# Optimization experiments

Measured on AMD Instinct MI355X. Metric: run time of the kernel, lower is better.

The kernel has to match this reference:

```python
import jax, jax.numpy as jnp
import numpy as np

# SMPL kinematic tree: parent[i] for joint i (root's parent is -1, unused)
PARENTS = [-1, 0, 0, 0, 1, 2, 3, 4, 5, 6, 7, 8, 9, 9, 9, 12, 13, 14, 16, 17, 18, 19, 20, 21]
NUM_JOINTS = 24
NUM_VERTS = 6890
BATCH = 128


def rodrigues(r):
    """r: [K,3] axis-angle -> [K,3,3] rotation (faithful to source, incl. cos(theta*pi)/sin(theta))."""
    eps = 1e-8
    theta = jnp.linalg.norm(r + eps, axis=-1, keepdims=True)  # [K,1]
    r_hat = r / theta                                          # [K,3]
    cos = jnp.cos(theta * jnp.pi)[..., None]                   # [K,1,1]
    sin = jnp.sin(theta)[..., None]                            # [K,1,1]
    rx, ry, rz = r_hat[:, 0], r_hat[:, 1], r_hat[:, 2]
    z = jnp.zeros_like(rx)
    m = jnp.stack([z, -rz, ry, rz, z, -rx, -ry, rx, z], axis=1).reshape(-1, 3, 3)
    eye = jnp.eye(3, dtype=r.dtype)
    dot = r_hat[:, :, None] * r_hat[:, None, :]                # outer product [K,3,3]
    return cos * eye + (1.0 - cos) * dot + sin * m


def setup_inputs() -> dict:
    key = jax.random.key(0)
    k1, k2, k3, k4 = jax.random.split(key, 4)
    V = jax.random.normal(k1, (BATCH, NUM_VERTS, 3), dtype=jnp.float32)
    J = jax.random.normal(k2, (BATCH, NUM_JOINTS, 3), dtype=jnp.float32)
    pose = jax.random.normal(k3, (BATCH, NUM_JOINTS, 3), dtype=jnp.float32)
    W = jax.random.uniform(k4, (BATCH, NUM_VERTS, NUM_JOINTS), dtype=jnp.float32)
    return {"V": V, "J": J, "pose": pose, "W": W}


def reference(V, J, pose, W):
    B = V.shape[0]
    M = NUM_JOINTS
    R = rodrigues(pose.reshape(-1, 3)).reshape(B, M, 3, 3)     # [B,M,3,3]
    # local translations: root uses J[0], others J[i] - J[parent[i]]
    par = np.array(PARENTS[1:])
    t = jnp.concatenate([J[:, :1], J[:, 1:] - J[:, par]], axis=1)  # [B,M,3]
    bottom = jnp.broadcast_to(jnp.array([0.0, 0.0, 0.0, 1.0], dtype=V.dtype), (B, M, 1, 4))
    A = jnp.concatenate([jnp.concatenate([R, t[..., None]], axis=-1), bottom], axis=2)  # [B,M,4,4]
    # forward kinematics along the tree (fixed 24-joint loop; parents always precede children)
    results = [A[:, 0]]
    for i in range(1, M):
        results.append(jnp.matmul(results[PARENTS[i]], A[:, i]))
    G = jnp.stack(results, axis=1)                              # [B,M,4,4]
    # subtract transformed rest-pose joint locations (the 'pack' correction)
    Jh = jnp.concatenate([J, jnp.zeros((B, M, 1), dtype=V.dtype)], axis=-1)  # [B,M,4]
    corr = jnp.einsum('bmij,bmj->bmi', G, Jh)                   # [B,M,4]
    Gc = G - jnp.concatenate([jnp.zeros((B, M, 4, 3), dtype=V.dtype), corr[..., None]], axis=-1)
    # linear blend skinning, without materializing [B,N,M,4,4]
    Tv = jnp.einsum('bnm,bmij->bnij', W, Gc)                    # [B,N,4,4]
    Vh = jnp.concatenate([V, jnp.ones((B, V.shape[1], 1), dtype=V.dtype)], axis=-1)  # [B,N,4]
    out = jnp.einsum('bnij,bnj->bni', Tv, Vh)                   # [B,N,4]
    return out[:, :, :3]
```

## Files before the change

### kernel.cpp

```cpp
#include <hip/hip_runtime.h>
#include <math.h>

#define NJ 24
#define NV 6890
#define NB 128

__constant__ int d_anc[NJ][8] = {
  {-1,-1,-1,-1,-1,-1,-1,-1},
  { 0,-1,-1,-1,-1,-1,-1,-1},
  { 0,-1,-1,-1,-1,-1,-1,-1},
  { 0,-1,-1,-1,-1,-1,-1,-1},
  { 1, 0,-1,-1,-1,-1,-1,-1},
  { 2, 0,-1,-1,-1,-1,-1,-1},
  { 3, 0,-1,-1,-1,-1,-1,-1},
  { 4, 1, 0,-1,-1,-1,-1,-1},
  { 5, 2, 0,-1,-1,-1,-1,-1},
  { 6, 3, 0,-1,-1,-1,-1,-1},
  { 7, 4, 1, 0,-1,-1,-1,-1},
  { 8, 5, 2, 0,-1,-1,-1,-1},
  { 9, 6, 3, 0,-1,-1,-1,-1},
  { 9, 6, 3, 0,-1,-1,-1,-1},
  { 9, 6, 3, 0,-1,-1,-1,-1},
  {12, 9, 6, 3, 0,-1,-1,-1},
  {13, 9, 6, 3, 0,-1,-1,-1},
  {14, 9, 6, 3, 0,-1,-1,-1},
  {16,13, 9, 6, 3, 0,-1,-1},
  {17,14, 9, 6, 3, 0,-1,-1},
  {18,16,13, 9, 6, 3, 0,-1},
  {19,17,14, 9, 6, 3, 0,-1},
  {20,18,16,13, 9, 6, 3, 0},
  {21,19,17,14, 9, 6, 3, 0}
};
__constant__ int d_par[NJ] = {-1,0,0,0,1,2,3,4,5,6,7,8,9,9,9,12,13,14,16,17,18,19,20,21};

__global__ __launch_bounds__(64) void chain_kernel(const float* __restrict__ J,
                                                   const float* __restrict__ pose,
                                                   float* __restrict__ Gc) {
    int b = blockIdx.x;
    int tid = threadIdx.x;
    __shared__ float A[NJ][12];

    if (tid < NJ) {
        int i = tid;
        const float* p = pose + ((size_t)b * NJ + i) * 3;
        float rx = p[0], ry = p[1], rz = p[2];
        float ex = rx + 1e-8f, ey = ry + 1e-8f, ez = rz + 1e-8f;
        float theta = sqrtf(ex * ex + ey * ey + ez * ez);
        float inv = 1.0f / theta;
        float hx = rx * inv, hy = ry * inv, hz = rz * inv;
        float c = cosf(theta * (float)M_PI);
        float s = sinf(theta);
        float oc = 1.0f - c;
        const float* jp = J + ((size_t)b * NJ + i) * 3;
        int par = d_par[i];
        float tx, ty, tz;
        if (par < 0) {
            tx = jp[0]; ty = jp[1]; tz = jp[2];
        } else {
            const float* jq = J + ((size_t)b * NJ + par) * 3;
            tx = jp[0] - jq[0]; ty = jp[1] - jq[1]; tz = jp[2] - jq[2];
        }
        A[i][0]  = c + oc * hx * hx;
        A[i][1]  = oc * hx * hy - s * hz;
        A[i][2]  = oc * hx * hz + s * hy;
        A[i][3]  = tx;
        A[i][4]  = oc * hy * hx + s * hz;
        A[i][5]  = c + oc * hy * hy;
        A[i][6]  = oc * hy * hz - s * hx;
        A[i][7]  = ty;
        A[i][8]  = oc * hz * hx - s * hy;
        A[i][9]  = oc * hz * hy + s * hx;
        A[i][10] = c + oc * hz * hz;
        A[i][11] = tz;
    }
    __syncthreads();

    if (tid < NJ) {
        int i = tid;
        float M[12];
        #pragma unroll
        for (int j = 0; j < 12; j++) M[j] = A[i][j];

        for (int k = 0; k < 8; k++) {
            int p = d_anc[i][k];
            if (p < 0) break;
            float P[12];
            #pragma unroll
            for (int j = 0; j < 12; j++) P[j] = A[p][j];
            float N[12];
            #pragma unroll
            for (int r = 0; r < 3; r++) {
                float p0 = P[r*4+0], p1 = P[r*4+1], p2 = P[r*4+2], p3 = P[r*4+3];
                N[r*4+0] = p0 * M[0] + p1 * M[4] + p2 * M[8];
                N[r*4+1] = p0 * M[1] + p1 * M[5] + p2 * M[9];
                N[r*4+2] = p0 * M[2] + p1 * M[6] + p2 * M[10];
                N[r*4+3] = p0 * M[3] + p1 * M[7] + p2 * M[11] + p3;
            }
            #pragma unroll
            for (int j = 0; j < 12; j++) M[j] = N[j];
        }

        const float* jp = J + ((size_t)b * NJ + i) * 3;
        float jx = jp[0], jy = jp[1], jz = jp[2];
        float* o = Gc + ((size_t)b * NJ + i) * 12;
        #pragma unroll
        for (int r = 0; r < 3; r++) {
            float g0 = M[r*4+0], g1 = M[r*4+1], g2 = M[r*4+2], g3 = M[r*4+3];
            float corr = g0 * jx + g1 * jy + g2 * jz;
            o[r*4+0] = g0;
            o[r*4+1] = g1;
            o[r*4+2] = g2;
            o[r*4+3] = g3 - corr;
        }
    }
}

typedef __attribute__((ext_vector_type(16))) float fx16;

__global__ __launch_bounds__(256) void lbs_kernel(const float* __restrict__ V,
                                                  const float* __restrict__ W,
                                                  const float* __restrict__ Gc,
                                                  float* __restrict__ out) {
    const int b = blockIdx.y;
    const int n = blockIdx.x * 256 + threadIdx.x;
    if (n >= NV) return;

    const float* gb = Gc + (size_t)b * (NJ * 12);

    const float4* wp = (const float4*)(W + ((size_t)b * NV + n) * 24);
    float4 warr[6];
    #pragma unroll
    for (int k = 0; k < 6; k++) warr[k] = wp[k];

    float T[12];
    #pragma unroll
    for (int j = 0; j < 12; j++) T[j] = 0.0f;

    #pragma unroll
    for (int c = 0; c < 6; c++) {
        fx16 ga, gB, gC;
        const float* p = gb + c * 48;
        asm volatile("s_load_dwordx16 %0, %3, 0x0\n\t"
                     "s_load_dwordx16 %1, %3, 0x40\n\t"
                     "s_load_dwordx16 %2, %3, 0x80\n\t"
                     "s_waitcnt lgkmcnt(0)"
                     : "=&s"(ga), "=&s"(gB), "=&s"(gC)
                     : "s"(p));

        const float wm[4] = {warr[c].x, warr[c].y, warr[c].z, warr[c].w};
        #pragma unroll
        for (int q = 0; q < 4; q++) {
            float wq = wm[q];
            #pragma unroll
            for (int j = 0; j < 12; j++) {
                const int flat = q * 12 + j;
                float g = (flat < 16) ? ga[flat < 16 ? flat : 0]
                        : (flat < 32) ? gB[flat >= 16 && flat < 32 ? flat - 16 : 0]
                                      : gC[flat >= 32 ? flat - 32 : 0];
                T[j] = fmaf(wq, g, T[j]);
            }
        }
    }

    const float* vp = V + ((size_t)b * NV + n) * 3;
    float vx = vp[0], vy = vp[1], vz = vp[2];
    float* op = out + ((size_t)b * NV + n) * 3;
    op[0] = T[0] * vx + T[1] * vy + T[2]  * vz + T[3];
    op[1] = T[4] * vx + T[5] * vy + T[6]  * vz + T[7];
    op[2] = T[8] * vx + T[9] * vy + T[10] * vz + T[11];
}

extern "C" void kernel_launch(void* const* d_in, const int* in_sizes, int n_in,
                              void* d_out, int out_size, void* d_ws, size_t ws_size,
                              hipStream_t stream) {
    const float* V    = (const float*)d_in[0];
    const float* J    = (const float*)d_in[1];
    const float* pose = (const float*)d_in[2];
    const float* W    = (const float*)d_in[3];
    float* out = (float*)d_out;
    float* Gc  = (float*)d_ws;

    chain_kernel<<<NB, 64, 0, stream>>>(J, pose, Gc);
    dim3 grid((NV + 255) / 256, NB);
    lbs_kernel<<<grid, 256, 0, stream>>>(V, W, Gc, out);
}
```

Baseline: 26.95 us.

## Transpose Gc to joint-minor layout and use packed FMA for skinning blend

The chain kernel now writes Gc transposed, element-major with joints contiguous, so each of the 12 transform entries holds 24 consecutive joint values. The skinning kernel then loads joint pairs from scalar registers and accumulates with v_pk_fma_f32, doing two joints per instruction and reducing the two lanes at the end. This aims to halve the VALU FMA count in the blend loop. It relies on packed FP32 FMA accepting SGPR pair operands, and it reorders the floating-point summation.

```diff
diff --git a/kernel.cpp b/kernel.cpp
--- a/kernel.cpp
+++ b/kernel.cpp
@@ -102,20 +102,27 @@
 
         const float* jp = J + ((size_t)b * NJ + i) * 3;
         float jx = jp[0], jy = jp[1], jz = jp[2];
-        float* o = Gc + ((size_t)b * NJ + i) * 12;
+        float* o = Gc + (size_t)b * 288;
         #pragma unroll
         for (int r = 0; r < 3; r++) {
             float g0 = M[r*4+0], g1 = M[r*4+1], g2 = M[r*4+2], g3 = M[r*4+3];
             float corr = g0 * jx + g1 * jy + g2 * jz;
-            o[r*4+0] = g0;
-            o[r*4+1] = g1;
-            o[r*4+2] = g2;
-            o[r*4+3] = g3 - corr;
+            o[(r*4+0)*24 + i] = g0;
+            o[(r*4+1)*24 + i] = g1;
+            o[(r*4+2)*24 + i] = g2;
+            o[(r*4+3)*24 + i] = g3 - corr;
         }
     }
 }
 
 typedef __attribute__((ext_vector_type(16))) float fx16;
+typedef __attribute__((ext_vector_type(2)))  float f2;
+
+__device__ __forceinline__ f2 mkf2(float a, float b) { f2 r; r.x = a; r.y = b; return r; }
+
+#define GPAIR(e) ((e) < 16 ? mkf2(gA[(e) & 15], gA[((e) + 1) & 15]) \
+                : (e) < 32 ? mkf2(gB[((e) - 16) & 15], gB[((e) - 15) & 15]) \
+                           : mkf2(gC[((e) - 32) & 15], gC[((e) - 31) & 15]))
 
 __global__ __launch_bounds__(256) void lbs_kernel(const float* __restrict__ V,
                                                   const float* __restrict__ W,
@@ -125,42 +132,50 @@
     const int n = blockIdx.x * 256 + threadIdx.x;
     if (n >= NV) return;
 
-    const float* gb = Gc + (size_t)b * (NJ * 12);
+    const float* gb = Gc + (size_t)b * 288;
 
     const float4* wp = (const float4*)(W + ((size_t)b * NV + n) * 24);
-    float4 warr[6];
-    #pragma unroll
-    for (int k = 0; k < 6; k++) warr[k] = wp[k];
-
-    float T[12];
-    #pragma unroll
-    for (int j = 0; j < 12; j++) T[j] = 0.0f;
+    float4 w4[6];
+    #pragma unroll
+    for (int k = 0; k < 6; k++) w4[k] = wp[k];
+    f2 wpr[12];
+    #pragma unroll
+    for (int k = 0; k < 6; k++) {
+        wpr[2 * k + 0] = mkf2(w4[k].x, w4[k].y);
+        wpr[2 * k + 1] = mkf2(w4[k].z, w4[k].w);
+    }
+
+    f2 T2[12];
+    #pragma unroll
+    for (int j = 0; j < 12; j++) T2[j] = mkf2(0.0f, 0.0f);
 
     #pragma unroll
     for (int c = 0; c < 6; c++) {
-        fx16 ga, gB, gC;
+        fx16 gA, gB, gC;
         const float* p = gb + c * 48;
         asm volatile("s_load_dwordx16 %0, %3, 0x0\n\t"
                      "s_load_dwordx16 %1, %3, 0x40\n\t"
                      "s_load_dwordx16 %2, %3, 0x80\n\t"
                      "s_waitcnt lgkmcnt(0)"
-                     : "=&s"(ga), "=&s"(gB), "=&s"(gC)
+                     : "=&s"(gA), "=&s"(gB), "=&s"(gC)
                      : "s"(p));
 
-        const float wm[4] = {warr[c].x, warr[c].y, warr[c].z, warr[c].w};
+        f2 TA = T2[2 * c + 0];
+        f2 TB = T2[2 * c + 1];
         #pragma unroll
-        for (int q = 0; q < 4; q++) {
-            float wq = wm[q];
-            #pragma unroll
-            for (int j = 0; j < 12; j++) {
-                const int flat = q * 12 + j;
-                float g = (flat < 16) ? ga[flat < 16 ? flat : 0]
-                        : (flat < 32) ? gB[flat >= 16 && flat < 32 ? flat - 16 : 0]
-                                      : gC[flat >= 32 ? flat - 32 : 0];
-                T[j] = fmaf(wq, g, T[j]);
-            }
-        }
-    }
+        for (int q = 0; q < 12; q++) {
+            f2 gpA = GPAIR(2 * q);
+            f2 gpB = GPAIR(24 + 2 * q);
+            asm("v_pk_fma_f32 %0, %1, %2, %0" : "+v"(TA) : "v"(wpr[q]), "s"(gpA));
+            asm("v_pk_fma_f32 %0, %1, %2, %0" : "+v"(TB) : "v"(wpr[q]), "s"(gpB));
+        }
+        T2[2 * c + 0] = TA;
+        T2[2 * c + 1] = TB;
+    }
+
+    float T[12];
+    #pragma unroll
+    for (int j = 0; j < 12; j++) T[j] = T2[j].x + T2[j].y;
 
     const float* vp = V + ((size_t)b * NV + n) * 3;
     float vx = vp[0], vy = vp[1], vz = vp[2];
```

Result: no change. 26.56 us (-1.5%).

## Process two vertices per thread with packed FMA and prefetched weights

Applied to the files above, without the earlier changes.

Each thread now skins two vertices 256 apart, so every scalar-loaded joint transform chunk is reused for both. The blend accumulation uses v_pk_fma_f32 on float pairs, and the next chunk of weights is loaded while the current one is processed. Vertex positions are loaded up front. This cuts scalar load and instruction overhead per vertex, at the cost of higher register pressure and half as many blocks.

```diff
diff --git a/kernel.cpp b/kernel.cpp
--- a/kernel.cpp
+++ b/kernel.cpp
@@ -116,58 +116,83 @@
 }
 
 typedef __attribute__((ext_vector_type(16))) float fx16;
+typedef __attribute__((ext_vector_type(2)))  float f2;
+
+__device__ __forceinline__ f2 mkf2(float a, float b) { f2 r; r.x = a; r.y = b; return r; }
+
+#define GPAIR(e) ((e) < 16 ? mkf2(gA[(e) & 15], gA[((e) + 1) & 15]) \
+                : (e) < 32 ? mkf2(gB[((e) - 16) & 15], gB[((e) - 15) & 15]) \
+                           : mkf2(gC[((e) - 32) & 15], gC[((e) - 31) & 15]))
 
 __global__ __launch_bounds__(256) void lbs_kernel(const float* __restrict__ V,
                                                   const float* __restrict__ W,
                                                   const float* __restrict__ Gc,
                                                   float* __restrict__ out) {
     const int b = blockIdx.y;
-    const int n = blockIdx.x * 256 + threadIdx.x;
-    if (n >= NV) return;
-
-    const float* gb = Gc + (size_t)b * (NJ * 12);
-
-    const float4* wp = (const float4*)(W + ((size_t)b * NV + n) * 24);
-    float4 warr[6];
+    const int tid = threadIdx.x;
+    const int n0 = blockIdx.x * 512 + tid;
+    if (n0 >= NV) return;
+    const int n1 = n0 + 256;
+    const bool has1 = (n1 < NV);
+    const int n1c = has1 ? n1 : n0;
+
+    const float* gb = Gc + (size_t)b * 288;
+    const float4* __restrict__ wp0 = (const float4*)(W + ((size_t)b * NV + n0) * 24);
+    const float4* __restrict__ wp1 = (const float4*)(W + ((size_t)b * NV + n1c) * 24);
+
+    const float* vp0 = V + ((size_t)b * NV + n0) * 3;
+    const float* vp1 = V + ((size_t)b * NV + n1c) * 3;
+    float v0x = vp0[0], v0y = vp0[1], v0z = vp0[2];
+    float v1x = vp1[0], v1y = vp1[1], v1z = vp1[2];
+
+    f2 Ta[6], Tb[6];
     #pragma unroll
-    for (int k = 0; k < 6; k++) warr[k] = wp[k];
-
-    float T[12];
-    #pragma unroll
-    for (int j = 0; j < 12; j++) T[j] = 0.0f;
+    for (int j = 0; j < 6; j++) { Ta[j] = mkf2(0.f, 0.f); Tb[j] = mkf2(0.f, 0.f); }
+
+    float4 wa = wp0[0];
+    float4 wb = wp1[0];
 
     #pragma unroll
     for (int c = 0; c < 6; c++) {
-        fx16 ga, gB, gC;
+        fx16 gA, gB, gC;
         const float* p = gb + c * 48;
         asm volatile("s_load_dwordx16 %0, %3, 0x0\n\t"
                      "s_load_dwordx16 %1, %3, 0x40\n\t"
                      "s_load_dwordx16 %2, %3, 0x80\n\t"
                      "s_waitcnt lgkmcnt(0)"
-                     : "=&s"(ga), "=&s"(gB), "=&s"(gC)
+                     : "=&s"(gA), "=&s"(gB), "=&s"(gC)
                      : "s"(p));
 
-        const float wm[4] = {warr[c].x, warr[c].y, warr[c].z, warr[c].w};
+        float4 wac = wa, wbc = wb;
+        if (c < 5) { wa = wp0[c + 1]; wb = wp1[c + 1]; }
+
+        const float wav[4] = {wac.x, wac.y, wac.z, wac.w};
+        const float wbv[4] = {wbc.x, wbc.y, wbc.z, wbc.w};
         #pragma unroll
         for (int q = 0; q < 4; q++) {
-            float wq = wm[q];
-            #pragma unroll
-            for (int j = 0; j < 12; j++) {
-                const int flat = q * 12 + j;
-                float g = (flat < 16) ? ga[flat < 16 ? flat : 0]
-                        : (flat < 32) ? gB[flat >= 16 && flat < 32 ? flat - 16 : 0]
-                                      : gC[flat >= 32 ? flat - 32 : 0];
-                T[j] = fmaf(wq, g, T[j]);
+            f2 wwa = mkf2(wav[q], wav[q]);
+            f2 wwb = mkf2(wbv[q], wbv[q]);
+            #pragma unroll
+            for (int e2 = 0; e2 < 6; e2++) {
+                f2 gp = GPAIR(q * 12 + 2 * e2);
+                asm("v_pk_fma_f32 %0, %1, %2, %0" : "+v"(Ta[e2]) : "v"(wwa), "s"(gp));
+                asm("v_pk_fma_f32 %0, %1, %2, %0" : "+v"(Tb[e2]) : "v"(wwb), "s"(gp));
             }
         }
     }
 
-    const float* vp = V + ((size_t)b * NV + n) * 3;
-    float vx = vp[0], vy = vp[1], vz = vp[2];
-    float* op = out + ((size_t)b * NV + n) * 3;
-    op[0] = T[0] * vx + T[1] * vy + T[2]  * vz + T[3];
-    op[1] = T[4] * vx + T[5] * vy + T[6]  * vz + T[7];
-    op[2] = T[8] * vx + T[9] * vy + T[10] * vz + T[11];
+    {
+        float* op = out + ((size_t)b * NV + n0) * 3;
+        op[0] = Ta[0].x * v0x + Ta[0].y * v0y + Ta[1].x * v0z + Ta[1].y;
+        op[1] = Ta[2].x * v0x + Ta[2].y * v0y + Ta[3].x * v0z + Ta[3].y;
+        op[2] = Ta[4].x * v0x + Ta[4].y * v0y + Ta[5].x * v0z + Ta[5].y;
+    }
+    if (has1) {
+        float* op = out + ((size_t)b * NV + n1) * 3;
+        op[0] = Tb[0].x * v1x + Tb[0].y * v1y + Tb[1].x * v1z + Tb[1].y;
+        op[1] = Tb[2].x * v1x + Tb[2].y * v1y + Tb[3].x * v1z + Tb[3].y;
+        op[2] = Tb[4].x * v1x + Tb[4].y * v1y + Tb[5].x * v1z + Tb[5].y;
+    }
 }
 
 extern "C" void kernel_launch(void* const* d_in, const int* in_sizes, int n_in,
@@ -181,6 +206,6 @@
     float* Gc  = (float*)d_ws;
 
     chain_kernel<<<NB, 64, 0, stream>>>(J, pose, Gc);
-    dim3 grid((NV + 255) / 256, NB);
+    dim3 grid((NV + 511) / 512, NB);
     lbs_kernel<<<grid, 256, 0, stream>>>(V, W, Gc, out);
 }
```

After: 38.17 us. 1.42x slower.

## Compute blend skinning weight-transform product with bf16 MFMA and LDS transpose

Applied to the files above, without the earlier changes.

Replaces per-thread scalar FMA accumulation of weighted joint transforms with 16x16x32 bf16 MFMA instructions, using W tiles as the A operand and the joint transform matrix as B. Results are staged through shared memory so each lane then applies its vertex's transform. Each block now processes 1024 vertices over four sequential groups. This trades fp32 accuracy for bf16 rounding of weights and transforms, and reduces the grid size, which may lower memory parallelism in a bandwidth-bound kernel.

```diff
diff --git a/kernel.cpp b/kernel.cpp
--- a/kernel.cpp
+++ b/kernel.cpp
@@ -1,5 +1,6 @@
 #include <hip/hip_runtime.h>
 #include <math.h>
+#include <string.h>
 
 #define NJ 24
 #define NV 6890
@@ -115,59 +116,97 @@
     }
 }
 
-typedef __attribute__((ext_vector_type(16))) float fx16;
+typedef __attribute__((ext_vector_type(8))) short bf16x8;
+typedef __attribute__((ext_vector_type(4))) float f32x4;
+
+__device__ __forceinline__ short f2bf(float f) {
+    unsigned int u;
+    memcpy(&u, &f, 4);
+    u += 0x7fffu + ((u >> 16) & 1u);
+    return (short)(u >> 16);
+}
+
+#define TLSTRIDE 20
 
 __global__ __launch_bounds__(256) void lbs_kernel(const float* __restrict__ V,
                                                   const float* __restrict__ W,
                                                   const float* __restrict__ Gc,
                                                   float* __restrict__ out) {
-    const int b = blockIdx.y;
-    const int n = blockIdx.x * 256 + threadIdx.x;
-    if (n >= NV) return;
+    const int b    = blockIdx.y;
+    const int wave = threadIdx.x >> 6;
+    const int lane = threadIdx.x & 63;
+    const int vwave = blockIdx.x * 1024 + wave * 256;
+    if (vwave >= NV) return;
+
+    __shared__ float tl[4 * 64 * TLSTRIDE];
+    float* mytl = &tl[wave * 64 * TLSTRIDE];
+
+    const int n16 = lane & 15;
+    const int g   = lane >> 4;
 
     const float* gb = Gc + (size_t)b * (NJ * 12);
-
-    const float4* wp = (const float4*)(W + ((size_t)b * NV + n) * 24);
-    float4 warr[6];
+    bf16x8 bfrag;
     #pragma unroll
-    for (int k = 0; k < 6; k++) warr[k] = wp[k];
-
-    float T[12];
-    #pragma unroll
-    for (int j = 0; j < 12; j++) T[j] = 0.0f;
-
-    #pragma unroll
-    for (int c = 0; c < 6; c++) {
-        fx16 ga, gB, gC;
-        const float* p = gb + c * 48;
-        asm volatile("s_load_dwordx16 %0, %3, 0x0\n\t"
-                     "s_load_dwordx16 %1, %3, 0x40\n\t"
-                     "s_load_dwordx16 %2, %3, 0x80\n\t"
-                     "s_waitcnt lgkmcnt(0)"
-                     : "=&s"(ga), "=&s"(gB), "=&s"(gC)
-                     : "s"(p));
-
-        const float wm[4] = {warr[c].x, warr[c].y, warr[c].z, warr[c].w};
+    for (int j = 0; j < 8; j++) {
+        const int k = 8 * g + j;
+        const float gval = (k < NJ && n16 < 12) ? gb[k * 12 + n16] : 0.0f;
+        bfrag[j] = f2bf(gval);
+    }
+
+    #pragma unroll 1
+    for (int grp = 0; grp < 4; grp++) {
+        const int gbase = vwave + grp * 64;
+
         #pragma unroll
-        for (int q = 0; q < 4; q++) {
-            float wq = wm[q];
-            #pragma unroll
-            for (int j = 0; j < 12; j++) {
-                const int flat = q * 12 + j;
-                float g = (flat < 16) ? ga[flat < 16 ? flat : 0]
-                        : (flat < 32) ? gB[flat >= 16 && flat < 32 ? flat - 16 : 0]
-                                      : gC[flat >= 32 ? flat - 32 : 0];
-                T[j] = fmaf(wq, g, T[j]);
+        for (int t = 0; t < 4; t++) {
+            const int tb = gbase + t * 16;
+            const int v  = tb + n16;
+            const int vc = v < NV ? v : NV - 1;
+
+            f32x4 lo = {0.f, 0.f, 0.f, 0.f}, hi = {0.f, 0.f, 0.f, 0.f};
+            if (g < 3) {
+                const float4* wp =
+                    (const float4*)(W + ((size_t)b * NV + vc) * 24 + g * 8);
+                float4 l4 = wp[0];
+                float4 h4 = wp[1];
+                lo[0] = l4.x; lo[1] = l4.y; lo[2] = l4.z; lo[3] = l4.w;
+                hi[0] = h4.x; hi[1] = h4.y; hi[2] = h4.z; hi[3] = h4.w;
             }
-        }
-    }
-
-    const float* vp = V + ((size_t)b * NV + n) * 3;
-    float vx = vp[0], vy = vp[1], vz = vp[2];
-    float* op = out + ((size_t)b * NV + n) * 3;
-    op[0] = T[0] * vx + T[1] * vy + T[2]  * vz + T[3];
-    op[1] = T[4] * vx + T[5] * vy + T[6]  * vz + T[7];
-    op[2] = T[8] * vx + T[9] * vy + T[10] * vz + T[11];
+            bf16x8 afrag;
+            #pragma unroll
+            for (int j = 0; j < 4; j++) afrag[j]     = f2bf(lo[j]);
+            #pragma unroll
+            for (int j = 0; j < 4; j++) afrag[4 + j] = f2bf(hi[j]);
+
+            f32x4 acc = {0.f, 0.f, 0.f, 0.f};
+            acc = __builtin_amdgcn_mfma_f32_16x16x32_bf16(afrag, bfrag, acc, 0, 0, 0);
+
+            #pragma unroll
+            for (int r = 0; r < 4; r++) {
+                const int lv = t * 16 + 4 * g + r;
+                mytl[lv * TLSTRIDE + n16] = acc[r];
+            }
+        }
+
+        __builtin_amdgcn_wave_barrier();
+
+        const int gv  = gbase + lane;
+        const int gvc = gv < NV ? gv : NV - 1;
+        const float* row = &mytl[lane * TLSTRIDE];
+        f32x4 t0 = *(const f32x4*)(row + 0);
+        f32x4 t1 = *(const f32x4*)(row + 4);
+        f32x4 t2 = *(const f32x4*)(row + 8);
+
+        const float* vp = V + ((size_t)b * NV + gvc) * 3;
+        const float vx = vp[0], vy = vp[1], vz = vp[2];
+        if (gv < NV) {
+            float* op = out + ((size_t)b * NV + gv) * 3;
+            op[0] = t0[0] * vx + t0[1] * vy + t0[2] * vz + t0[3];
+            op[1] = t1[0] * vx + t1[1] * vy + t1[2] * vz + t1[3];
+            op[2] = t2[0] * vx + t2[1] * vy + t2[2] * vz + t2[3];
+        }
+        __builtin_amdgcn_wave_barrier();
+    }
 }
 
 extern "C" void kernel_launch(void* const* d_in, const int* in_sizes, int n_in,
@@ -181,6 +220,6 @@
     float* Gc  = (float*)d_ws;
 
     chain_kernel<<<NB, 64, 0, stream>>>(J, pose, Gc);
-    dim3 grid((NV + 255) / 256, NB);
+    dim3 grid((NV + 1023) / 1024, NB);
     lbs_kernel<<<grid, 256, 0, stream>>>(V, W, Gc, out);
 }
```

Result: no change. 26.52 us (-1.6%).
